# Kernel optimization log

Hardware: AMD Instinct MI355X
Metric: run time of the kernel (lower is better)

## Reference

```python
import jax, jax.numpy as jnp
import numpy as np

N = 100000   # nodes per layer
E = 600000   # edges per block
FIN = 256    # raw feature dim
H = 128      # hidden_size
C = 47       # n_classes
L = 3        # num_layers = n_layers + 1
NOUT = 10000 # seed nodes
GEN_EPS = 1e-7
T = 1.0
LN_EPS = 1e-5


def setup_inputs() -> dict:
    key = jax.random.key(0)
    ks = jax.random.split(key, 10)
    return {
        "x": jax.random.normal(ks[0], (N, FIN), jnp.float32),
        "src": jax.random.randint(ks[1], (L - 1, E), 0, N),
        "dst": jax.random.randint(ks[2], (L - 1, E), 0, N),
        "node_map": jax.random.randint(ks[3], (L - 1, N), 0, N),
        "final_map": jax.random.randint(ks[4], (NOUT,), 0, N),
        "enc_w": jax.random.normal(ks[5], (FIN, H), jnp.float32) * 0.05,
        "enc_b": jnp.zeros((H,), jnp.float32),
        "gcn_w": jax.random.normal(ks[6], (L, H, H), jnp.float32) * 0.05,
        "gcn_b": jnp.zeros((L, H), jnp.float32),
        "ln_g": jnp.ones((L, H), jnp.float32),
        "ln_b": jnp.zeros((L, H), jnp.float32),
        "pred_w": jax.random.normal(ks[7], (H, C), jnp.float32) * 0.05,
        "pred_b": jnp.zeros((C,), jnp.float32),
    }


def _layer_norm(h, g, b):
    mu = jnp.mean(h, axis=-1, keepdims=True)
    var = jnp.mean(jnp.square(h - mu), axis=-1, keepdims=True)
    return (h - mu) * jax.lax.rsqrt(var + LN_EPS) * g + b


def _gen_conv(h, src, dst, w, b):
    # GENConv, aggr='softmax', mlp_layers=1, no edge_attr, no msg_norm.
    m = jax.nn.relu(h[src]) + GEN_EPS                      # [E, H] messages
    # per-destination, per-feature segment softmax with temperature T
    mx = jax.ops.segment_max(m * T, dst, num_segments=N)   # [N, H]
    e = jnp.exp(m * T - mx[dst])                           # [E, H]
    denom = jax.ops.segment_sum(e, dst, num_segments=N)    # [N, H]
    alpha = e / (denom[dst] + 1e-16)
    agg = jax.ops.segment_sum(m * alpha, dst, num_segments=N)  # [N, H]
    return (agg + h) @ w + b                               # residual + Linear (MLP)


def reference(x, src, dst, node_map, final_map, enc_w, enc_b,
              gcn_w, gcn_b, ln_g, ln_b, pred_w, pred_b):
    h = x @ enc_w + enc_b                                  # node_features_encoder
    h = _gen_conv(h, src[0], dst[0], gcn_w[0], gcn_b[0])   # gcns[0] with block-0 edges
    for layer in range(1, L):                              # res+ block
        h2 = jax.nn.relu(_layer_norm(h, ln_g[layer - 1], ln_b[layer - 1]))
        # dropout is identity in eval mode (p applied with training=False)
        # gcns[layer] uses the edge_index set BEFORE this iteration's move
        h = _gen_conv(h2, src[layer - 1], dst[layer - 1],
                      gcn_w[layer], gcn_b[layer]) + h
        h = h[node_map[layer - 1]]                         # nf_move_layer_to gather
    h = jax.nn.relu(_layer_norm(h, ln_g[L - 1], ln_b[L - 1]))
    h = h @ pred_w + pred_b                                # node_pred_linear
    h = h[final_map]                                       # seed-node extraction
    return jax.nn.log_softmax(h, axis=-1)
```

## Files before the change

### kernel.cpp

```cpp
#include <hip/hip_runtime.h>
#include <hip/hip_bf16.h>
#include <hip/hip_fp16.h>

typedef unsigned short u16;
typedef unsigned int u32;

#define N_NODES 100000
#define N_EDGES 600000
#define FIN_D   256
#define HDIM    128
#define NCLS    47
#define NOUT_D  10000
#define NCHUNK  196
#define NP2     100352
#define PCH     2048
#define PNB     ((N_EDGES + PCH - 1) / PCH)

typedef short bf16x8 __attribute__((ext_vector_type(8)));
typedef float f32x4  __attribute__((ext_vector_type(4)));

#define GPTR(p) (const __attribute__((address_space(1))) u32*)(p)
#define LPTR(p) (__attribute__((address_space(3))) u32*)(p)

__device__ __forceinline__ float bf2f(u16 u) {
    union { u32 i; float f; } v; v.i = ((u32)u) << 16; return v.f;
}
__device__ __forceinline__ u16 f2bf(float f) {
    __hip_bfloat16 h = __float2bfloat16(f);
    return *reinterpret_cast<u16*>(&h);
}
__device__ __forceinline__ float loadF(const void* p, size_t i, bool f32) {
    if (f32) return ((const float*)p)[i];
    return bf2f(((const u16*)p)[i]);
}
__device__ __forceinline__ float wave_sum(float v) {
    #pragma unroll
    for (int o = 32; o > 0; o >>= 1) v += __shfl_xor(v, o, 64);
    return v;
}
__device__ __forceinline__ float wave_max(float v) {
    #pragma unroll
    for (int o = 32; o > 0; o >>= 1) v = fmaxf(v, __shfl_xor(v, o, 64));
    return v;
}
__device__ __forceinline__ int wave_sum_i(int v) {
    #pragma unroll
    for (int o = 32; o > 0; o >>= 1) v += __shfl_xor(v, o, 64);
    return v;
}
__device__ __forceinline__ int block_excl_scan_256(int v, int* wsum) {
    int lane = threadIdx.x & 63, wv = threadIdx.x >> 6;
    int inc = v;
    #pragma unroll
    for (int off = 1; off < 64; off <<= 1) {
        int u = __shfl_up(inc, off, 64);
        if (lane >= off) inc += u;
    }
    if (lane == 63) wsum[wv] = inc;
    __syncthreads();
    if (threadIdx.x == 0) {
        int a = 0;
        #pragma unroll
        for (int w = 0; w < 4; ++w) { int t = wsum[w]; wsum[w] = a; a += t; }
    }
    __syncthreads();
    return inc - v + wsum[wv];
}

__global__ __launch_bounds__(256) void dtype_detect_kernel(
    const u16* __restrict__ x, int* __restrict__ flag)
{
    int i = blockIdx.x * 256 + threadIdx.x;
    u32 e = (x[i] >> 7) & 0xFF;
    unsigned long long b = __ballot(e >= 200);
    if ((threadIdx.x & 63) == 0) {
        int c = __popcll(b);
        if (c) atomicAdd(&flag[1], c);
    }
}

__global__ __launch_bounds__(256) void hist2_kernel(
    const int* __restrict__ dst, int* __restrict__ deg2, int egrid)
{
    int half = (blockIdx.x >= egrid) ? 1 : 0;
    int e = (blockIdx.x - half * egrid) * 256 + threadIdx.x;
    if (e < N_EDGES) atomicAdd(&deg2[half * NP2 + dst[half * N_EDGES + e]], 1);
}

__global__ __launch_bounds__(256) void csum2_kernel(
    const int* __restrict__ deg2, int* __restrict__ csum)
{
    __shared__ int ws[4];
    int half = (blockIdx.x >= NCHUNK) ? 1 : 0;
    int b = blockIdx.x - half * NCHUNK;
    int i0 = half * NP2 + b * 512 + threadIdx.x;
    int v = 0;
    if (b * 512 + threadIdx.x < N_NODES) v += deg2[i0];
    if (b * 512 + threadIdx.x + 256 < N_NODES) v += deg2[i0 + 256];
    v = wave_sum_i(v);
    int lane = threadIdx.x & 63, wv = threadIdx.x >> 6;
    if (lane == 0) ws[wv] = v;
    __syncthreads();
    if (threadIdx.x == 0)
        csum[blockIdx.x] = ws[0] + ws[1] + ws[2] + ws[3];
}

__global__ __launch_bounds__(256) void coff2_kernel(
    const int* __restrict__ csum, int* __restrict__ coff,
    int* __restrict__ bcur)
{
    __shared__ int wsum[4];
    int t = threadIdx.x;
    for (int h = 0; h < 2; ++h) {
        int v = (t < NCHUNK) ? csum[h * NCHUNK + t] : 0;
        int excl = block_excl_scan_256(v, wsum);
        if (t < NCHUNK) {
            coff[h * NCHUNK + t] = excl;
            bcur[(h * NCHUNK + t) * 16] = excl;
        }
        __syncthreads();
    }
}

__global__ __launch_bounds__(256) void scan2_kernel(
    const int* __restrict__ deg2, const int* __restrict__ coff,
    int* __restrict__ rp0, int* __restrict__ rp1)
{
    __shared__ int wsum[4];
    int half = (blockIdx.x >= NCHUNK) ? 1 : 0;
    int b = blockIdx.x - half * NCHUNK;
    const int* deg = deg2 + half * NP2;
    int* rp = half ? rp1 : rp0;
    int t = threadIdx.x;
    int i0 = b * 512 + 2 * t;
    int d0 = (i0 < N_NODES) ? deg[i0] : 0;
    int d1 = (i0 + 1 < N_NODES) ? deg[i0 + 1] : 0;
    int excl = block_excl_scan_256(d0 + d1, wsum);
    int base = coff[half * NCHUNK + b] + excl;
    if (i0 < N_NODES)     rp[i0] = base;
    if (i0 + 1 < N_NODES) rp[i0 + 1] = base + d0;
    if (b == 0 && t == 0) rp[N_NODES] = N_EDGES;
}

__global__ __launch_bounds__(256) void bucket_part_kernel(
    const int* __restrict__ src, const int* __restrict__ dst,
    const int* __restrict__ comp1,
    int* __restrict__ bcur, int2* __restrict__ tmp)
{
    __shared__ int hist[NCHUNK];
    __shared__ int base[NCHUNK];
    int half = (blockIdx.x >= PNB) ? 1 : 0;
    int b = blockIdx.x - half * PNB;
    int e0 = b * PCH;
    for (int i = threadIdx.x; i < NCHUNK; i += 256) hist[i] = 0;
    __syncthreads();

    int2 loc[8];
    #pragma unroll
    for (int t = 0; t < 8; ++t) {
        int e = e0 + t * 256 + threadIdx.x;
        loc[t].y = -1;
        if (e < N_EDGES) {
            int ge = half * N_EDGES + e;
            int d = dst[ge];
            int s = src[ge];
            if (half) s = comp1[s];
            loc[t] = make_int2(s, d);
            atomicAdd(&hist[d >> 9], 1);
        }
    }
    __syncthreads();
    for (int i = threadIdx.x; i < NCHUNK; i += 256) {
        int h = hist[i];
        base[i] = (h > 0) ? atomicAdd(&bcur[(half * NCHUNK + i) * 16], h) : 0;
        hist[i] = 0;
    }
    __syncthreads();
    #pragma unroll
    for (int t = 0; t < 8; ++t) {
        if (loc[t].y >= 0) {
            int bk = loc[t].y >> 9;
            int pos = base[bk] + atomicAdd(&hist[bk], 1);
            tmp[(size_t)half * N_EDGES + pos] = loc[t];
        }
    }
}

__global__ __launch_bounds__(256) void bucket_sort_kernel(
    const int2* __restrict__ tmp,
    const int* __restrict__ rp0, const int* __restrict__ rp1,
    const int* __restrict__ coff, const int* __restrict__ csum,
    int* __restrict__ ei0, int* __restrict__ ei1)
{
    __shared__ int cur[512];
    int half = (blockIdx.x >= NCHUNK) ? 1 : 0;
    int b = blockIdx.x - half * NCHUNK;
    const int* rp = half ? rp1 : rp0;
    int* ei = half ? ei1 : ei0;
    int n0 = b * 512;
    #pragma unroll
    for (int i = threadIdx.x; i < 512; i += 256) {
        int n = n0 + i;
        cur[i] = (n < N_NODES) ? rp[n] : 0;
    }
    __syncthreads();
    int beg = coff[half * NCHUNK + b];
    int end = beg + csum[half * NCHUNK + b];
    for (int i = beg + threadIdx.x; i < end; i += 256) {
        int2 p = tmp[(size_t)half * N_EDGES + i];
        int pos = atomicAdd(&cur[p.y & 511], 1);
        ei[pos] = p.x;
    }
}

__global__ __launch_bounds__(256) void pack_b_kernel(
    const void* __restrict__ enc_w, const void* __restrict__ gcn_w,
    const int* __restrict__ dt, u16* __restrict__ Bp)
{
    const bool f32 = (dt[1] > 16);
    int o = blockIdx.x * 256 + threadIdx.x;
    if (o >= 32768 + 3 * 16384) return;
    const void* srcp; size_t soff; int m;
    if (o < 32768) { srcp = enc_w; soff = 0; m = o; }
    else {
        int l = (o - 32768) >> 14;
        srcp = gcn_w; soff = (size_t)l * 16384; m = (o - 32768) & 16383;
    }
    int j    = m & 7;
    int lane = (m >> 3) & 63;
    int ct   = (m >> 9) & 7;
    int kidx = m >> 12;
    int k = kidx * 32 + (lane >> 4) * 8 + j;
    int n = ct * 16 + (lane & 15);
    Bp[o] = f2bf(loadF(srcp, soff + (size_t)k * HDIM + n, f32));
}

__global__ __launch_bounds__(256, 2) void enc_gemm_kernel(
    const void* __restrict__ Araw, const u16* __restrict__ Bp,
    const void* __restrict__ bias, const int* __restrict__ dt,
    u16* __restrict__ OutBF)
{
    extern __shared__ char SH[];
    const bool f32 = (dt[1] > 16);
    const int tid  = threadIdx.x;
    const int w    = tid >> 6;
    const int lane = tid & 63;
    const int quad = lane >> 4;
    const int cl   = lane & 15;
    const int m0   = blockIdx.x * 16;

    #pragma unroll
    for (int i = 0; i < 16; ++i) {
        int off = (w * 16 + i) * 1024;
        __builtin_amdgcn_global_load_lds(
            GPTR((const char*)Bp + off + lane * 16),
            LPTR(SH + off), 16, 0, 0);
    }
    if (f32) {
        #pragma unroll
        for (int i = 0; i < 4; ++i) {
            int row = w * 4 + i;
            int src = (lane * 16) ^ ((row & 7) << 4);
            __builtin_amdgcn_global_load_lds(
                GPTR((const char*)Araw + (size_t)(m0 + row) * 1024 + src),
                LPTR(SH + 65536 + row * 1024), 16, 0, 0);
        }
    } else {
        #pragma unroll
        for (int i = 0; i < 2; ++i) {
            int r0 = (w * 2 + i) * 2;
            int row = r0 + (lane >> 5);
            int src = ((lane & 31) * 16) ^ ((row & 7) << 4);
            __builtin_amdgcn_global_load_lds(
                GPTR((const char*)Araw + (size_t)(m0 + row) * 512 + src),
                LPTR(SH + 65536 + r0 * 512), 16, 0, 0);
        }
    }

    f32x4 acc[2];
    acc[0] = (f32x4){0.f, 0.f, 0.f, 0.f};
    acc[1] = (f32x4){0.f, 0.f, 0.f, 0.f};
    const int ct0 = w * 2;
    const int swz = (cl & 7) << 4;

    __syncthreads();

    #pragma unroll
    for (int k = 0; k < 8; ++k) {
        bf16x8 av;
        if (f32) {
            const char* rb = SH + 65536 + cl * 1024;
            int lo = (k * 128 + quad * 32) ^ swz;
            float4 v0 = *(const float4*)(rb + lo);
            float4 v1 = *(const float4*)(rb + (lo ^ 16));
            union { u32 u[4]; bf16x8 v; } cv;
            cv.u[0] = (u32)f2bf(v0.x) | ((u32)f2bf(v0.y) << 16);
            cv.u[1] = (u32)f2bf(v0.z) | ((u32)f2bf(v0.w) << 16);
            cv.u[2] = (u32)f2bf(v1.x) | ((u32)f2bf(v1.y) << 16);
            cv.u[3] = (u32)f2bf(v1.z) | ((u32)f2bf(v1.w) << 16);
            av = cv.v;
        } else {
            const char* rb = SH + 65536 + cl * 512;
            av = *(const bf16x8*)(rb + ((k * 64 + quad * 16) ^ swz));
        }
        #pragma unroll
        for (int c = 0; c < 2; ++c) {
            bf16x8 b = *(const bf16x8*)(SH + k * 8192 + (ct0 + c) * 1024 + lane * 16);
            acc[c] = __builtin_amdgcn_mfma_f32_16x16x32_bf16(av, b, acc[c], 0, 0, 0);
        }
    }

    #pragma unroll
    for (int reg = 0; reg < 4; ++reg) {
        int grow = m0 + quad * 4 + reg;
        #pragma unroll
        for (int c = 0; c < 2; ++c) {
            int col = (ct0 + c) * 16 + cl;
            float v = acc[c][reg] + loadF(bias, col, f32);
            OutBF[(size_t)grow * HDIM + col] = f2bf(v);
        }
    }
}

template<bool OWN_MAP>
__global__ __launch_bounds__(256) void agg_msg_kernel(
    const int* __restrict__ rp, const int* __restrict__ eidx,
    const u16* __restrict__ HBin, const int* __restrict__ own_map,
    u16* __restrict__ Amsg)
{
    __shared__ u32 RS[4][16][64];
    int wave = threadIdx.x >> 6;
    int lane = threadIdx.x & 63;
    int n = blockIdx.x * 4 + wave;
    if (n >= N_NODES) return;
    const u32* HB32 = (const u32*)HBin;
    int nn = OWN_MAP ? own_map[n] : n;
    u32 own = HB32[(size_t)nn * 64 + lane];
    int beg = rp[n], end = rp[n + 1];
    float den0 = 0.f, den1 = 0.f, num0 = 0.f, num1 = 0.f;
    for (int c = beg; c < end; c += 16) {
        int cnt = end - c; if (cnt > 16) cnt = 16;
        int e = c + (lane & 15); if (e > end - 1) e = end - 1;
        int ei = eidx[e];
        int nI = (cnt + 3) >> 2;
        #pragma unroll
        for (int i = 0; i < 4; ++i) {
            if (i < nI) {
                int s = __shfl(ei, i * 4 + (lane >> 4), 64);
                __builtin_amdgcn_global_load_lds(
                    GPTR((const char*)HBin + (size_t)s * 256 + (lane & 15) * 16),
                    LPTR(&RS[wave][i * 4][0]), 16, 0, 0);
            }
        }
        asm volatile("s_waitcnt vmcnt(0)" ::: "memory");
        __builtin_amdgcn_sched_barrier(0);
        #pragma unroll
        for (int t = 0; t < 16; ++t) {
            if (t >= cnt) break;
            u32 h = RS[wave][t][lane];
            float m0 = fmaxf(bf2f((u16)(h & 0xffff)), 0.f) + 1e-7f;
            float m1 = fmaxf(bf2f((u16)(h >> 16)),    0.f) + 1e-7f;
            float e0 = __expf(m0), e1 = __expf(m1);
            den0 += e0; num0 += m0 * e0;
            den1 += e1; num1 += m1 * e1;
        }
        asm volatile("s_waitcnt lgkmcnt(0)" ::: "memory");
        __builtin_amdgcn_sched_barrier(0);
    }
    float a0 = num0 / (den0 + 1e-16f) + bf2f((u16)(own & 0xffff));
    float a1 = num1 / (den1 + 1e-16f) + bf2f((u16)(own >> 16));
    ((u32*)Amsg)[(size_t)n * 64 + lane] = (u32)f2bf(a0) | ((u32)f2bf(a1) << 16);
}

template<bool RES, bool OWN_MAP, bool WRITE_LN>
__global__ __launch_bounds__(256) void conv_gemm_kernel(
    const u16* __restrict__ Amsg, const int* __restrict__ own_map,
    const u16* __restrict__ Bp, int Bpbase,
    const void* __restrict__ bias, int biasoff,
    const __half* __restrict__ Resid,
    const void* __restrict__ lng, const void* __restrict__ lnb, int lnoff,
    const int* __restrict__ dt,
    __half* __restrict__ OutH, u16* __restrict__ HBout)
{
    const bool f32 = (dt[1] > 16);
    __shared__ u16 Bsh[16384];
    __shared__ u16 Ash[8192];
    const int tid  = threadIdx.x;
    const int w    = tid >> 6;
    const int lane = tid & 63;
    const int quad = lane >> 4;
    const int cl   = lane & 15;
    const int m0   = blockIdx.x * 64;

    {
        const char* Bp2 = (const char*)(Bp + Bpbase);
        #pragma unroll
        for (int i = 0; i < 8; ++i)
            __builtin_amdgcn_global_load_lds(
                GPTR(Bp2 + i * 4096 + w * 1024 + lane * 16),
                LPTR((char*)Bsh + i * 4096 + w * 1024), 16, 0, 0);
        const char* Ab = (const char*)Amsg + (size_t)m0 * 256;
        #pragma unroll
        for (int i = 0; i < 4; ++i) {
            int row_local = i * 16 + w * 4 + (lane >> 4);
            int off = ((lane & 15) * 16) ^ ((row_local & 7) << 4);
            __builtin_amdgcn_global_load_lds(
                GPTR(Ab + (size_t)row_local * 256 + off),
                LPTR((char*)Ash + i * 4096 + w * 1024), 16, 0, 0);
        }
    }

    __syncthreads();

    const int row_local = w * 16 + cl;
    const char* ar = (const char*)Ash + row_local * 256;
    const int akey = (row_local & 7) << 4;
    bf16x8 afr[4];
    #pragma unroll
    for (int kidx = 0; kidx < 4; ++kidx)
        afr[kidx] = *(const bf16x8*)(ar + ((kidx * 64 + quad * 16) ^ akey));

    f32x4 acc[8];
    #pragma unroll
    for (int ct = 0; ct < 8; ++ct) acc[ct] = (f32x4){0.f, 0.f, 0.f, 0.f};
    #pragma unroll
    for (int kidx = 0; kidx < 4; ++kidx) {
        const u16* bb = Bsh + ((size_t)(kidx * 8) * 64 + lane) * 8;
        #pragma unroll
        for (int ct = 0; ct < 8; ++ct) {
            bf16x8 b = *(const bf16x8*)(bb + (size_t)ct * 512);
            acc[ct] = __builtin_amdgcn_mfma_f32_16x16x32_bf16(afr[kidx], b, acc[ct], 0, 0, 0);
        }
    }

    #pragma unroll
    for (int reg = 0; reg < 4; ++reg) {
        int n = m0 + w * 16 + quad * 4 + reg;
        if (n >= N_NODES) continue;
        size_t rrow = 0;
        if (RES) rrow = (size_t)(OWN_MAP ? own_map[n] : n) * HDIM;
        float v[8];
        float s1 = 0.f, s2 = 0.f;
        #pragma unroll
        for (int ct = 0; ct < 8; ++ct) {
            int col = ct * 16 + cl;
            float x = acc[ct][reg] + loadF(bias, biasoff + col, f32);
            if (RES) x += __half2float(Resid[rrow + col]);
            v[ct] = x;
            OutH[(size_t)n * HDIM + col] = __float2half(x);
            s1 += x; s2 += x * x;
        }
        if (WRITE_LN) {
            #pragma unroll
            for (int o = 1; o < 16; o <<= 1) {
                s1 += __shfl_xor(s1, o, 64);
                s2 += __shfl_xor(s2, o, 64);
            }
            float mu = s1 * (1.0f / 128.0f);
            float var = s2 * (1.0f / 128.0f) - mu * mu;
            float rs = rsqrtf(fmaxf(var, 0.f) + 1e-5f);
            #pragma unroll
            for (int ct = 0; ct < 8; ++ct) {
                int col = ct * 16 + cl;
                float y = fmaxf((v[ct] - mu) * rs * loadF(lng, lnoff + col, f32)
                                + loadF(lnb, lnoff + col, f32), 0.f);
                HBout[(size_t)n * HDIM + col] = f2bf(y);
            }
        }
    }
}

__global__ __launch_bounds__(64) void final_head_kernel(
    const __half* __restrict__ Hsrc, const int* __restrict__ map1,
    const int* __restrict__ fmap,
    const void* __restrict__ g, const void* __restrict__ b, int goff,
    const void* __restrict__ pw, const void* __restrict__ pb,
    const int* __restrict__ dt, void* __restrict__ out)
{
    const bool f32 = (dt[1] > 16);
    __shared__ float sh[HDIM];
    int i = blockIdx.x;
    int lane = threadIdx.x;
    int jj = map1[fmap[i]];
    __half2 hv = *((const __half2*)(Hsrc + (size_t)jj * HDIM) + lane);
    float2 v = __half22float2(hv);
    float mu = wave_sum(v.x + v.y) * (1.0f / 128.0f);
    float d0 = v.x - mu, d1 = v.y - mu;
    float var = wave_sum(d0 * d0 + d1 * d1) * (1.0f / 128.0f);
    float rs = rsqrtf(var + 1e-5f);
    int f0 = lane * 2;
    sh[f0]     = fmaxf(d0 * rs * loadF(g, goff + f0, f32)     + loadF(b, goff + f0, f32),     0.0f);
    sh[f0 + 1] = fmaxf(d1 * rs * loadF(g, goff + f0 + 1, f32) + loadF(b, goff + f0 + 1, f32), 0.0f);
    __syncthreads();
    float acc = -1e30f;
    if (lane < NCLS) {
        acc = loadF(pb, lane, f32);
        #pragma unroll 4
        for (int k = 0; k < HDIM; ++k)
            acc = fmaf(sh[k], loadF(pw, k * NCLS + lane, f32), acc);
    }
    float mx = wave_max(acc);
    float ex = (lane < NCLS) ? __expf(acc - mx) : 0.0f;
    float sum = wave_sum(ex);
    if (lane < NCLS) {
        float r = acc - mx - logf(sum);
        if (f32) ((float*)out)[(size_t)i * NCLS + lane] = r;
        else     ((u16*)out)[(size_t)i * NCLS + lane] = f2bf(r);
    }
}

extern "C" void kernel_launch(void* const* d_in, const int* in_sizes, int n_in,
                              void* d_out, int out_size, void* d_ws, size_t ws_size,
                              hipStream_t stream) {
    const void* x       = d_in[0];
    const int* src      = (const int*)d_in[1];
    const int* dst      = (const int*)d_in[2];
    const int* node_map = (const int*)d_in[3];
    const int* fmap     = (const int*)d_in[4];
    const void* enc_w   = d_in[5];
    const void* enc_b   = d_in[6];
    const void* gcn_w   = d_in[7];
    const void* gcn_b   = d_in[8];
    const void* ln_g    = d_in[9];
    const void* ln_b    = d_in[10];
    const void* pred_w  = d_in[11];
    const void* pred_b  = d_in[12];

    char* ws = (char*)d_ws;
    const size_t szH = (size_t)N_NODES * HDIM * sizeof(u16);
    __half* Pa  = (__half*)ws;  ws += szH;
    __half* Pb  = (__half*)ws;  ws += szH;
    u16*   HBa  = (u16*)ws;     ws += szH;
    u16*   HBb  = (u16*)ws;     ws += szH;
    u16*   Amsg = (u16*)ws;     ws += szH;
    int*   FLAG = (int*)ws;     ws += 1024;
    u16*   Bp   = (u16*)ws;     ws += (size_t)(32768 + 3 * 16384) * 2 + 1024;
    int*  deg2  = (int*)ws;  ws += (size_t)2 * NP2 * 4;
    int*  rp0   = (int*)ws;  ws += (size_t)(N_NODES + 2) * 4;
    int*  rp1   = (int*)ws;  ws += (size_t)(N_NODES + 2) * 4;
    int*  ei0   = (int*)ws;  ws += (size_t)N_EDGES * 4;
    int*  ei1   = (int*)ws;  ws += (size_t)N_EDGES * 4;
    int2* tmp   = (int2*)ws; ws += (size_t)2 * N_EDGES * 8;
    int*  csum  = (int*)ws;  ws += 2048;
    int*  coff  = (int*)ws;  ws += 2048;
    int*  bcur  = (int*)ws;  ws += (size_t)2 * NCHUNK * 16 * 4 + 1024;

    dim3 blk(256);
    const int ggrid = (N_NODES + 63) / 64;
    const int g16   = (N_NODES + 15) / 16;
    const int egrid = (N_EDGES + 255) / 256;
    const int agrid = (N_NODES + 3) / 4;
    const int pgrid = (32768 + 3 * 16384 + 255) / 256;

    hipMemsetAsync(FLAG, 0, 64, stream);
    dtype_detect_kernel<<<256, blk, 0, stream>>>((const u16*)x, FLAG);
    pack_b_kernel<<<pgrid, blk, 0, stream>>>(enc_w, gcn_w, FLAG, Bp);

    hipMemsetAsync(deg2, 0, (size_t)2 * NP2 * 4, stream);
    hist2_kernel<<<2 * egrid, blk, 0, stream>>>(dst, deg2, egrid);
    csum2_kernel<<<2 * NCHUNK, blk, 0, stream>>>(deg2, csum);
    coff2_kernel<<<1, blk, 0, stream>>>(csum, coff, bcur);
    scan2_kernel<<<2 * NCHUNK, blk, 0, stream>>>(deg2, coff, rp0, rp1);
    bucket_part_kernel<<<2 * PNB, blk, 0, stream>>>(src, dst, node_map, bcur, tmp);
    bucket_sort_kernel<<<2 * NCHUNK, blk, 0, stream>>>(tmp, rp0, rp1, coff, csum,
                                                       ei0, ei1);

    enc_gemm_kernel<<<g16, blk, 81920, stream>>>(x, Bp, enc_b, FLAG, HBa);

    agg_msg_kernel<false><<<agrid, blk, 0, stream>>>(rp0, ei0, HBa, nullptr, Amsg);
    conv_gemm_kernel<false, false, true><<<ggrid, blk, 0, stream>>>(
        Amsg, nullptr, Bp, 32768, gcn_b, 0, nullptr,
        ln_g, ln_b, 0, FLAG, Pa, HBb);

    agg_msg_kernel<false><<<agrid, blk, 0, stream>>>(rp0, ei0, HBb, nullptr, Amsg);
    conv_gemm_kernel<true, false, true><<<ggrid, blk, 0, stream>>>(
        Amsg, nullptr, Bp, 32768 + 16384, gcn_b, 128, Pa,
        ln_g, ln_b, 128, FLAG, Pb, HBa);

    agg_msg_kernel<true><<<agrid, blk, 0, stream>>>(rp1, ei1, HBa, node_map, Amsg);
    conv_gemm_kernel<true, true, false><<<ggrid, blk, 0, stream>>>(
        Amsg, node_map, Bp, 32768 + 2 * 16384, gcn_b, 256, Pb,
        ln_g, ln_b, 256, FLAG, Pa, nullptr);

    final_head_kernel<<<NOUT_D, dim3(64), 0, stream>>>(
        Pa, node_map + N_NODES, fmap, ln_g, ln_b, 256, pred_w, pred_b, FLAG,
        (void*)d_out);
}
```

Measured before the change: 571.2 us.

## Stage prediction weights in LDS for final head; split encoder GEMM launch

The final head kernel now processes four seed nodes per 256-thread block and first stages pred_w and pred_b into shared memory (padded to 48 columns). The dot product then reads LDS instead of issuing strided global loads per class. Separately, the encoder GEMM is split into two launches of half the rows each via a new rowbase argument, which adds launch overhead for no clear gain. Each head block now re-reads the full weight matrix, which adds global traffic per block in exchange for faster inner loops.

```diff
diff --git a/kernel.cpp b/kernel.cpp
--- a/kernel.cpp
+++ b/kernel.cpp
@@ -238,7 +238,7 @@
 __global__ __launch_bounds__(256, 2) void enc_gemm_kernel(
     const void* __restrict__ Araw, const u16* __restrict__ Bp,
     const void* __restrict__ bias, const int* __restrict__ dt,
-    u16* __restrict__ OutBF)
+    int rowbase, u16* __restrict__ OutBF)
 {
     extern __shared__ char SH[];
     const bool f32 = (dt[1] > 16);
@@ -247,7 +247,7 @@
     const int lane = tid & 63;
     const int quad = lane >> 4;
     const int cl   = lane & 15;
-    const int m0   = blockIdx.x * 16;
+    const int m0   = rowbase + blockIdx.x * 16;
 
     #pragma unroll
     for (int i = 0; i < 16; ++i) {
@@ -470,7 +470,7 @@
     }
 }
 
-__global__ __launch_bounds__(64) void final_head_kernel(
+__global__ __launch_bounds__(256) void final_head_kernel(
     const __half* __restrict__ Hsrc, const int* __restrict__ map1,
     const int* __restrict__ fmap,
     const void* __restrict__ g, const void* __restrict__ b, int goff,
@@ -478,9 +478,17 @@
     const int* __restrict__ dt, void* __restrict__ out)
 {
     const bool f32 = (dt[1] > 16);
-    __shared__ float sh[HDIM];
-    int i = blockIdx.x;
-    int lane = threadIdx.x;
+    __shared__ float pwl[HDIM * 48];
+    __shared__ float pbl[64];
+    __shared__ float sh[4][HDIM];
+    const int tid = threadIdx.x, wave = tid >> 6, lane = tid & 63;
+
+    for (int i = tid; i < HDIM * NCLS; i += 256)
+        pwl[(i / NCLS) * 48 + (i % NCLS)] = loadF(pw, i, f32);
+    if (tid < NCLS) pbl[tid] = loadF(pb, tid, f32);
+    __syncthreads();
+
+    int i = blockIdx.x * 4 + wave;
     int jj = map1[fmap[i]];
     __half2 hv = *((const __half2*)(Hsrc + (size_t)jj * HDIM) + lane);
     float2 v = __half22float2(hv);
@@ -489,15 +497,14 @@
     float var = wave_sum(d0 * d0 + d1 * d1) * (1.0f / 128.0f);
     float rs = rsqrtf(var + 1e-5f);
     int f0 = lane * 2;
-    sh[f0]     = fmaxf(d0 * rs * loadF(g, goff + f0, f32)     + loadF(b, goff + f0, f32),     0.0f);
-    sh[f0 + 1] = fmaxf(d1 * rs * loadF(g, goff + f0 + 1, f32) + loadF(b, goff + f0 + 1, f32), 0.0f);
-    __syncthreads();
+    sh[wave][f0]     = fmaxf(d0 * rs * loadF(g, goff + f0, f32)     + loadF(b, goff + f0, f32),     0.0f);
+    sh[wave][f0 + 1] = fmaxf(d1 * rs * loadF(g, goff + f0 + 1, f32) + loadF(b, goff + f0 + 1, f32), 0.0f);
     float acc = -1e30f;
     if (lane < NCLS) {
-        acc = loadF(pb, lane, f32);
-        #pragma unroll 4
+        acc = pbl[lane];
+        #pragma unroll 8
         for (int k = 0; k < HDIM; ++k)
-            acc = fmaf(sh[k], loadF(pw, k * NCLS + lane, f32), acc);
+            acc = fmaf(sh[wave][k], pwl[k * 48 + lane], acc);
     }
     float mx = wave_max(acc);
     float ex = (lane < NCLS) ? __expf(acc - mx) : 0.0f;
@@ -547,7 +554,7 @@
 
     dim3 blk(256);
     const int ggrid = (N_NODES + 63) / 64;
-    const int g16   = (N_NODES + 15) / 16;
+    const int gHALF = 3125;
     const int egrid = (N_EDGES + 255) / 256;
     const int agrid = (N_NODES + 3) / 4;
     const int pgrid = (32768 + 3 * 16384 + 255) / 256;
@@ -565,7 +572,8 @@
     bucket_sort_kernel<<<2 * NCHUNK, blk, 0, stream>>>(tmp, rp0, rp1, coff, csum,
                                                        ei0, ei1);
 
-    enc_gemm_kernel<<<g16, blk, 81920, stream>>>(x, Bp, enc_b, FLAG, HBa);
+    enc_gemm_kernel<<<gHALF, blk, 81920, stream>>>(x, Bp, enc_b, FLAG, 0, HBa);
+    enc_gemm_kernel<<<gHALF, blk, 81920, stream>>>(x, Bp, enc_b, FLAG, 50000, HBa);
 
     agg_msg_kernel<false><<<agrid, blk, 0, stream>>>(rp0, ei0, HBa, nullptr, Amsg);
     conv_gemm_kernel<false, false, true><<<ggrid, blk, 0, stream>>>(
@@ -582,7 +590,7 @@
         Amsg, node_map, Bp, 32768 + 2 * 16384, gcn_b, 256, Pb,
         ln_g, ln_b, 256, FLAG, Pa, nullptr);
 
-    final_head_kernel<<<NOUT_D, dim3(64), 0, stream>>>(
+    final_head_kernel<<<NOUT_D / 4, blk, 0, stream>>>(
         Pa, node_map + N_NODES, fmap, ln_g, ln_b, 256, pred_w, pred_b, FLAG,
         (void*)d_out);
 }
```

Result: no change. 574.0 us (+0.5%).
